# Performance work log

Hardware: AMD Instinct MI355X
Metric: run time of the kernel (lower is better)

Reference implementation:

```python
import jax, jax.numpy as jnp
import numpy as np

# Sparse pattern from the original torch.sparse_coo_tensor indices:
# 5 diagonal entries plus the (0,4) and (4,0) corners.
_ROWS = jnp.array([0, 1, 2, 3, 4, 0, 4], dtype=jnp.int32)
_COLS = jnp.array([0, 1, 2, 3, 4, 4, 0], dtype=jnp.int32)


def setup_inputs() -> dict:
    key = jax.random.key(0)
    k1, k2 = jax.random.split(key)
    X = jax.random.normal(k1, (7,), dtype=jnp.float32)   # learned parameter values
    A = jax.random.normal(k2, (5, 5), dtype=jnp.float32)  # forward input
    return {"X": X, "A": A}


def reference(X, A):
    # X_full = scatter(X into 5x5 at sparse pattern) + I
    eye = jnp.eye(5, dtype=X.dtype)
    X_full = eye.at[_ROWS, _COLS].add(X)
    # sum((solve(X_full, A) - I)^2)
    diff = jnp.linalg.solve(X_full, A) - eye
    return jnp.sum(diff * diff)
```

## Files before the change

### kernel.cpp

```cpp
#include <hip/hip_runtime.h>
#include <hip/hip_bf16.h>


__global__ void Invert_36129264894624_kernel(const float* __restrict__ X,
                                             const float* __restrict__ A,
                                             float* __restrict__ out) {
    if (threadIdx.x != 0 || blockIdx.x != 0) return;

    const int rows[7] = {0, 1, 2, 3, 4, 0, 4};
    const int cols[7] = {0, 1, 2, 3, 4, 4, 0};

    float M[5][5];
    #pragma unroll
    for (int i = 0; i < 5; ++i)
        #pragma unroll
        for (int j = 0; j < 5; ++j)
            M[i][j] = (i == j) ? 1.0f : 0.0f;
    #pragma unroll
    for (int k = 0; k < 7; ++k)
        M[rows[k]][cols[k]] += X[k];

    float B[5][5];
    #pragma unroll
    for (int i = 0; i < 5; ++i)
        #pragma unroll
        for (int j = 0; j < 5; ++j)
            B[i][j] = A[i * 5 + j];

    for (int c = 0; c < 5; ++c) {
        int p = c;
        float best = fabsf(M[c][c]);
        for (int r = c + 1; r < 5; ++r) {
            float v = fabsf(M[r][c]);
            if (v > best) { best = v; p = r; }
        }
        if (p != c) {
            for (int j = 0; j < 5; ++j) {
                float t = M[c][j]; M[c][j] = M[p][j]; M[p][j] = t;
                t = B[c][j]; B[c][j] = B[p][j]; B[p][j] = t;
            }
        }
        float inv = 1.0f / M[c][c];
        for (int j = 0; j < 5; ++j) { M[c][j] *= inv; B[c][j] *= inv; }
        for (int r = 0; r < 5; ++r) {
            if (r == c) continue;
            float f = M[r][c];
            for (int j = 0; j < 5; ++j) {
                M[r][j] = __builtin_fmaf(-f, M[c][j], M[r][j]);
                B[r][j] = __builtin_fmaf(-f, B[c][j], B[r][j]);
            }
        }
    }

    float s = 0.0f;
    #pragma unroll
    for (int i = 0; i < 5; ++i)
        #pragma unroll
        for (int j = 0; j < 5; ++j) {
            float d = B[i][j] - ((i == j) ? 1.0f : 0.0f);
            s += d * d;
        }

    out[0] = s;
}

extern "C" void kernel_launch(void* const* d_in, const int* in_sizes, int n_in,
                              void* d_out, int out_size, void* d_ws, size_t ws_size,
                              hipStream_t stream) {
    const float* X = (const float*)d_in[0];
    const float* A = (const float*)d_in[1];
    float* out = (float*)d_out;
    Invert_36129264894624_kernel<<<1, 64, 0, stream>>>(X, A, out);
}
```

Measured before the change: 11.29 us.

## Replace generic Gauss-Jordan solve with closed-form block solve for fixed sparsity

Exploits the fixed sparsity structure, three decoupled diagonal entries plus a 2x2 block on rows and columns 0 and 4, to solve the system in closed form. A 2x2 inverse and scalar reciprocals replace the pivoting elimination loop. Hardware approximate reciprocals (rcp) are used instead of IEEE division. Pivoting is dropped, and the approximate reciprocal can cost some accuracy.

```diff
diff --git a/kernel.cpp b/kernel.cpp
--- a/kernel.cpp
+++ b/kernel.cpp
@@ -7,59 +7,47 @@
                                              float* __restrict__ out) {
     if (threadIdx.x != 0 || blockIdx.x != 0) return;
 
-    const int rows[7] = {0, 1, 2, 3, 4, 0, 4};
-    const int cols[7] = {0, 1, 2, 3, 4, 4, 0};
+    const float d0 = 1.0f + X[0];
+    const float d1 = 1.0f + X[1];
+    const float d2 = 1.0f + X[2];
+    const float d3 = 1.0f + X[3];
+    const float d4 = 1.0f + X[4];
+    const float a  = X[5];
+    const float b  = X[6];
 
-    float M[5][5];
-    #pragma unroll
-    for (int i = 0; i < 5; ++i)
-        #pragma unroll
-        for (int j = 0; j < 5; ++j)
-            M[i][j] = (i == j) ? 1.0f : 0.0f;
-    #pragma unroll
-    for (int k = 0; k < 7; ++k)
-        M[rows[k]][cols[k]] += X[k];
-
-    float B[5][5];
-    #pragma unroll
-    for (int i = 0; i < 5; ++i)
-        #pragma unroll
-        for (int j = 0; j < 5; ++j)
-            B[i][j] = A[i * 5 + j];
-
-    for (int c = 0; c < 5; ++c) {
-        int p = c;
-        float best = fabsf(M[c][c]);
-        for (int r = c + 1; r < 5; ++r) {
-            float v = fabsf(M[r][c]);
-            if (v > best) { best = v; p = r; }
-        }
-        if (p != c) {
-            for (int j = 0; j < 5; ++j) {
-                float t = M[c][j]; M[c][j] = M[p][j]; M[p][j] = t;
-                t = B[c][j]; B[c][j] = B[p][j]; B[p][j] = t;
-            }
-        }
-        float inv = 1.0f / M[c][c];
-        for (int j = 0; j < 5; ++j) { M[c][j] *= inv; B[c][j] *= inv; }
-        for (int r = 0; r < 5; ++r) {
-            if (r == c) continue;
-            float f = M[r][c];
-            for (int j = 0; j < 5; ++j) {
-                M[r][j] = __builtin_fmaf(-f, M[c][j], M[r][j]);
-                B[r][j] = __builtin_fmaf(-f, B[c][j], B[r][j]);
-            }
-        }
-    }
+    const float det  = __builtin_fmaf(d0, d4, -a * b);
+    const float rdet = __builtin_amdgcn_rcpf(det);
+    const float r1   = __builtin_amdgcn_rcpf(d1);
+    const float r2   = __builtin_amdgcn_rcpf(d2);
+    const float r3   = __builtin_amdgcn_rcpf(d3);
 
     float s = 0.0f;
     #pragma unroll
-    for (int i = 0; i < 5; ++i)
-        #pragma unroll
-        for (int j = 0; j < 5; ++j) {
-            float d = B[i][j] - ((i == j) ? 1.0f : 0.0f);
-            s += d * d;
-        }
+    for (int j = 0; j < 5; ++j) {
+        const float a0 = A[0 * 5 + j];
+        const float a1 = A[1 * 5 + j];
+        const float a2 = A[2 * 5 + j];
+        const float a3 = A[3 * 5 + j];
+        const float a4 = A[4 * 5 + j];
+
+        const float y0 = (__builtin_fmaf(d4, a0, -a * a4)) * rdet;
+        const float y1 = a1 * r1;
+        const float y2 = a2 * r2;
+        const float y3 = a3 * r3;
+        const float y4 = (__builtin_fmaf(d0, a4, -b * a0)) * rdet;
+
+        const float e0 = y0 - (j == 0 ? 1.0f : 0.0f);
+        const float e1 = y1 - (j == 1 ? 1.0f : 0.0f);
+        const float e2 = y2 - (j == 2 ? 1.0f : 0.0f);
+        const float e3 = y3 - (j == 3 ? 1.0f : 0.0f);
+        const float e4 = y4 - (j == 4 ? 1.0f : 0.0f);
+
+        s = __builtin_fmaf(e0, e0, s);
+        s = __builtin_fmaf(e1, e1, s);
+        s = __builtin_fmaf(e2, e2, s);
+        s = __builtin_fmaf(e3, e3, s);
+        s = __builtin_fmaf(e4, e4, s);
+    }
 
     out[0] = s;
 }
```

Result: faster. 9.808 us (-13.1%).
